# Kernel tuning notes

Measured on AMD Instinct MI355X. Metric: run time of the kernel, lower is better.

Reference implementation:

```python
import jax, jax.numpy as jnp
import numpy as np

KN = 4        # kernel_number
K = 3         # kernel size
CIN = 256
COUT = 256
BN_EPS = 1e-5


def _rotation_matrices(thetas):
    """thetas: [b, n] -> rot mats [b, n, 9, 9] (faithful port of _get_rotation_matrix)."""
    b, n = thetas.shape
    t = thetas.reshape(-1)                      # [b*n]
    x = jnp.cos(t); y = jnp.sin(t)
    a = x - y; bxy = x * y; c = x + y
    z = jnp.zeros_like(t); o = jnp.ones_like(t)
    pos = [
        [a, 1 - a, z, z, z, z, z, z, z],
        [z, x - bxy, bxy, z, 1 - c + bxy, y - bxy, z, z, z],
        [z, z, a, z, z, 1 - a, z, z, z],
        [bxy, y - bxy, z, x - bxy, 1 - c + bxy, z, z, z, z],
        [z, z, z, z, o, z, z, z, z],
        [z, z, z, z, 1 - c + bxy, x - bxy, z, y - bxy, bxy],
        [z, z, z, 1 - a, z, z, a, z, z],
        [z, z, z, y - bxy, 1 - c + bxy, z, bxy, x - bxy, z],
        [z, z, z, z, z, z, z, 1 - a, a],
    ]
    neg = [
        [c, z, z, 1 - c, z, z, z, z, z],
        [-bxy, x + bxy, z, bxy - y, 1 - a - bxy, z, z, z, z],
        [z, 1 - c, c, z, z, z, z, z, z],
        [z, z, z, x + bxy, 1 - a - bxy, z, -bxy, bxy - y, z],
        [z, z, z, z, o, z, z, z, z],
        [z, bxy - y, -bxy, z, 1 - a - bxy, x + bxy, z, z, z],
        [z, z, z, z, z, z, c, 1 - c, z],
        [z, z, z, z, 1 - a - bxy, bxy - y, z, x + bxy, -bxy],
        [z, z, z, z, z, 1 - c, z, z, c],
    ]
    P = jnp.stack([jnp.stack(r, 0) for r in pos], 0)    # [9, 9, b*n]
    N = jnp.stack([jnp.stack(r, 0) for r in neg], 0)    # [9, 9, b*n]
    R = jnp.where(t >= 0, P, N)                          # [9, 9, b*n]
    return R.transpose(2, 0, 1).reshape(b, n, K * K, K * K)


def _rotate_weights(weights, lambdas, thetas):
    """weights [n, Cout, Cin, 3, 3], lambdas/thetas [b, n] -> [b*Cout, Cin, 3, 3]."""
    b, n = thetas.shape
    _, Cout, Cin, _, _ = weights.shape
    rot = _rotation_matrices(thetas) * lambdas[:, :, None, None]   # [b, n, 9, 9]
    rot = rot.transpose(0, 2, 1, 3).reshape(b * K * K, n * K * K)  # [b*9, n*9]
    w = weights.transpose(0, 3, 4, 1, 2).reshape(n * K * K, Cout * Cin)
    w = rot @ w                                                    # [b*9, Cout*Cin]
    w = w.reshape(b, K, K, Cout, Cin).transpose(0, 3, 4, 1, 2)
    return w.reshape(b * Cout, Cin, K, K)


def _forward(x, weight, w_lambda, w_theta, bn_gamma, bn_beta, bn_mean, bn_var):
    b, Cin, H, W = x.shape
    Cout = weight.shape[1]
    # routing: GAP -> linear heads (sigmoid for lambdas, softsign*pi for thetas)
    pooled = x.mean(axis=(2, 3))                        # [b, Cin]
    lambdas = jax.nn.sigmoid(pooled @ w_lambda)         # [b, n]
    thetas = jax.nn.soft_sign(pooled @ w_theta) * jnp.pi  # [b, n]
    # per-sample rotated weights + grouped conv (groups = b)
    rw = _rotate_weights(weight, lambdas, thetas)       # [b*Cout, Cin, 3, 3]
    xr = x.reshape(1, b * Cin, H, W)
    out = jax.lax.conv_general_dilated(
        xr, rw, window_strides=(1, 1), padding=((1, 1), (1, 1)),
        dimension_numbers=('NCHW', 'OIHW', 'NCHW'), feature_group_count=b)
    out = out.reshape(b, Cout, H, W)
    # BatchNorm (inference, running stats) + ReLU
    inv = jax.lax.rsqrt(bn_var + BN_EPS)
    out = (out - bn_mean[None, :, None, None]) * (inv * bn_gamma)[None, :, None, None] \
          + bn_beta[None, :, None, None]
    return jax.nn.relu(out)


def setup_inputs() -> dict:
    key = jax.random.key(0)
    ks = jax.random.split(key, 8)
    B, H, W = 16, 64, 64
    x = jax.random.normal(ks[0], (B, CIN, H, W), dtype=jnp.float32)
    fan_in = CIN * K * K
    weight = jax.random.normal(ks[1], (KN, COUT, CIN, K, K), dtype=jnp.float32) * np.sqrt(2.0 / fan_in)
    w_lambda = jax.random.normal(ks[2], (CIN, KN), dtype=jnp.float32) * np.sqrt(2.0 / CIN)
    w_theta = jax.random.normal(ks[3], (CIN, KN), dtype=jnp.float32) * np.sqrt(2.0 / CIN)
    bn_gamma = jax.random.uniform(ks[4], (COUT,), dtype=jnp.float32, minval=0.5, maxval=1.5)
    bn_beta = jax.random.normal(ks[5], (COUT,), dtype=jnp.float32) * 0.1
    bn_mean = jax.random.normal(ks[6], (COUT,), dtype=jnp.float32) * 0.1
    bn_var = jax.random.uniform(ks[7], (COUT,), dtype=jnp.float32, minval=0.5, maxval=1.5)
    return {'x': x, 'weight': weight, 'w_lambda': w_lambda, 'w_theta': w_theta,
            'bn_gamma': bn_gamma, 'bn_beta': bn_beta, 'bn_mean': bn_mean, 'bn_var': bn_var}


def reference(x, weight, w_lambda, w_theta, bn_gamma, bn_beta, bn_mean, bn_var):
    return _forward(x, weight, w_lambda, w_theta, bn_gamma, bn_beta, bn_mean, bn_var)
```

## Files before the change

### kernel.cpp

```cpp
#include <hip/hip_runtime.h>
#include <math.h>

typedef __bf16  bf16x8 __attribute__((ext_vector_type(8)));
typedef float   f32x4  __attribute__((ext_vector_type(4)));

#define GLD_LDS16(dst, src)                                                      \
    __builtin_amdgcn_global_load_lds(                                            \
        (const __attribute__((address_space(1))) unsigned int*)(src),            \
        (__attribute__((address_space(3))) unsigned int*)(dst), 16, 0, 0)

__global__ __launch_bounds__(256) void transpose_kernel(const float* __restrict__ x,
                                                        __bf16* __restrict__ xT,
                                                        float* __restrict__ pooled) {
    __shared__ unsigned int lp[128][68];
    const int h = blockIdx.x, b = blockIdx.y;
    const int t = threadIdx.x;
    if (h == 0 && b == 0) {
        for (int i = t; i < 4096; i += 256) pooled[i] = 0.f;
    }
    const int w4 = t & 15;
#pragma unroll
    for (int k = 0; k < 8; ++k) {
        int ci2 = k * 16 + (t >> 4);
        int ci  = ci2 * 2;
        const float4 a = *(const float4*)(x + (((size_t)(b * 256 + ci    ) * 64 + h) * 64 + w4 * 4));
        const float4 c = *(const float4*)(x + (((size_t)(b * 256 + ci + 1) * 64 + h) * 64 + w4 * 4));
        union { __bf16 hh[2]; unsigned int u; } p0, p1, p2, p3;
        p0.hh[0] = (__bf16)a.x; p0.hh[1] = (__bf16)c.x;
        p1.hh[0] = (__bf16)a.y; p1.hh[1] = (__bf16)c.y;
        p2.hh[0] = (__bf16)a.z; p2.hh[1] = (__bf16)c.z;
        p3.hh[0] = (__bf16)a.w; p3.hh[1] = (__bf16)c.w;
        uint4 v = {p0.u, p1.u, p2.u, p3.u};
        *(uint4*)&lp[ci2][w4 * 4] = v;
    }
    __syncthreads();
    const int w = t >> 2, q = t & 3;
    __bf16* dst = xT + (((size_t)b * 64 + h) * 64 + w) * 256 + q * 64;
#pragma unroll
    for (int j = 0; j < 8; ++j) {
        int c0 = q * 32 + j * 4;
        uint4 v;
        v.x = lp[c0 + 0][w];
        v.y = lp[c0 + 1][w];
        v.z = lp[c0 + 2][w];
        v.w = lp[c0 + 3][w];
        *(uint4*)(dst + j * 8) = v;
    }
}

__global__ __launch_bounds__(256) void pool_kernel(const __bf16* __restrict__ xT,
                                                   float* __restrict__ pooled) {
    int blk = blockIdx.x;
    int b = blk >> 4, s = blk & 15;
    int t = threadIdx.x;
    int oc  = (t & 31) << 3;
    int hw0 = t >> 5;
    float a8[8];
#pragma unroll
    for (int j = 0; j < 8; j++) a8[j] = 0.f;
    const __bf16* base = xT + (((size_t)b * 4096 + s * 256 + hw0) * 256) + oc;
#pragma unroll 4
    for (int i = 0; i < 32; ++i) {
        bf16x8 v = *(const bf16x8*)(base + (size_t)i * 8 * 256);
#pragma unroll
        for (int j = 0; j < 8; j++) a8[j] += (float)v[j];
    }
    __shared__ float red[256][8];
#pragma unroll
    for (int j = 0; j < 8; j++) red[t][j] = a8[j];
    __syncthreads();
    if (t < 32) {
#pragma unroll
        for (int j = 0; j < 8; j++) {
            float s8 = 0.f;
#pragma unroll
            for (int g = 0; g < 8; g++) s8 += red[g * 32 + t][j];
            atomicAdd(&pooled[b * 256 + t * 8 + j], s8 * (1.f / 4096.f));
        }
    }
}

__global__ __launch_bounds__(64) void routing_kernel(
    const float* __restrict__ pooled, const float* __restrict__ w_lambda,
    const float* __restrict__ w_theta, float* __restrict__ slg) {
    int t = threadIdx.x;
    int b = t >> 2, n = t & 3;
    float zl = 0.f, zt = 0.f;
    for (int ci = 0; ci < 256; ci++) {
        float p = pooled[b * 256 + ci];
        zl += p * w_lambda[ci * 4 + n];
        zt += p * w_theta[ci * 4 + n];
    }
    float lam = 1.f / (1.f + expf(-zl));
    float th  = 3.14159265358979323846f * (zt / (1.f + fabsf(zt)));
    float xc = cosf(th), ys = sinf(th);
    float a = xc - ys, bb = xc * ys, c = xc + ys;
    float R[9][9];
#pragma unroll
    for (int i = 0; i < 9; i++)
#pragma unroll
        for (int j = 0; j < 9; j++) R[i][j] = 0.f;
    if (th >= 0.f) {
        R[0][0] = a;       R[0][1] = 1 - a;
        R[1][1] = xc - bb; R[1][2] = bb;       R[1][4] = 1 - c + bb; R[1][5] = ys - bb;
        R[2][2] = a;       R[2][5] = 1 - a;
        R[3][0] = bb;      R[3][1] = ys - bb;  R[3][3] = xc - bb;    R[3][4] = 1 - c + bb;
        R[4][4] = 1.f;
        R[5][4] = 1 - c + bb; R[5][5] = xc - bb; R[5][7] = ys - bb;  R[5][8] = bb;
        R[6][3] = 1 - a;   R[6][6] = a;
        R[7][3] = ys - bb; R[7][4] = 1 - c + bb; R[7][6] = bb;       R[7][7] = xc - bb;
        R[8][7] = 1 - a;   R[8][8] = a;
    } else {
        R[0][0] = c;       R[0][3] = 1 - c;
        R[1][0] = -bb;     R[1][1] = xc + bb;  R[1][3] = bb - ys;    R[1][4] = 1 - a - bb;
        R[2][1] = 1 - c;   R[2][2] = c;
        R[3][3] = xc + bb; R[3][4] = 1 - a - bb; R[3][6] = -bb;      R[3][7] = bb - ys;
        R[4][4] = 1.f;
        R[5][1] = bb - ys; R[5][2] = -bb;      R[5][4] = 1 - a - bb; R[5][5] = xc + bb;
        R[6][6] = c;       R[6][7] = 1 - c;
        R[7][4] = 1 - a - bb; R[7][5] = bb - ys; R[7][7] = xc + bb;  R[7][8] = -bb;
        R[8][5] = 1 - c;   R[8][8] = c;
    }
    float* o = slg + ((size_t)(b * 4 + n) * 9) * 12;
#pragma unroll
    for (int p = 0; p < 9; p++) {
#pragma unroll
        for (int q = 0; q < 9; q++) o[p * 12 + q] = lam * R[p][q];
        o[p * 12 + 9] = o[p * 12 + 10] = o[p * 12 + 11] = 0.f;
    }
}

__global__ __launch_bounds__(256) void rotw_kernel(
    const float* __restrict__ weight, const float* __restrict__ slg,
    __bf16* __restrict__ rwq) {
    __shared__ __attribute__((aligned(16))) float sl[16][4][9][12];
    __shared__ float wlds[4][2304];
    int co = blockIdx.x;
    int t = threadIdx.x;
#pragma unroll
    for (int n = 0; n < 4; n++) {
        const float* wp = weight + ((size_t)n * 256 + co) * 2304;
        for (int i = t; i < 2304; i += 256) wlds[n][i] = wp[i];
    }
    for (int i = t; i < 1728; i += 256)
        ((float4*)sl)[i] = ((const float4*)slg)[i];
    __syncthreads();
    int ci = t;
    float4 wa[4], wb[4];
    float  wc[4];
#pragma unroll
    for (int n = 0; n < 4; n++) {
        const float* wp = &wlds[n][ci * 9];
        wa[n] = make_float4(wp[0], wp[1], wp[2], wp[3]);
        wb[n] = make_float4(wp[4], wp[5], wp[6], wp[7]);
        wc[n] = wp[8];
    }
    for (int b = 0; b < 16; b++) {
#pragma unroll
        for (int p = 0; p < 9; p++) {
            float s = 0.f;
#pragma unroll
            for (int n = 0; n < 4; n++) {
                float4 sa = *(const float4*)&sl[b][n][p][0];
                float4 sb = *(const float4*)&sl[b][n][p][4];
                float  sc = sl[b][n][p][8];
                s += sa.x * wa[n].x + sa.y * wa[n].y + sa.z * wa[n].z + sa.w * wa[n].w
                   + sb.x * wb[n].x + sb.y * wb[n].y + sb.z * wb[n].z + sb.w * wb[n].w
                   + sc * wc[n];
            }
            rwq[(((size_t)b * 9 + p) * 256 + co) * 256 + ci] = (__bf16)s;
        }
    }
}

__global__ __launch_bounds__(256, 2) void conv_kernel(
    const __bf16* __restrict__ xT, const __bf16* __restrict__ rwq,
    const float* __restrict__ bn_gamma, const float* __restrict__ bn_beta,
    const float* __restrict__ bn_mean,  const float* __restrict__ bn_var,
    float* __restrict__ out) {
    __shared__ __attribute__((aligned(16))) __bf16 xs[10][4][66][8];
    __shared__ __attribute__((aligned(16))) __bf16 as9[9][4][66][8];
    __shared__ float bns[64], bnh[64];

    const int t    = threadIdx.x;
    const int lane = t & 63;
    const int wv   = t >> 6;
    const int l15  = lane & 15;
    const int kq4  = lane >> 4;

    const int lin  = blockIdx.x;
    const int r    = lin & 7;
    const int k    = lin >> 3;
    const int b    = (r << 1) | (k >> 5);
    const int inner = k & 31;
    const int co0  = (inner & 3) << 6;
    const int h0   = (inner >> 2) << 3;

    if (t < 64) {
        float inv = rsqrtf(bn_var[co0 + t] + 1e-5f);
        float sc = bn_gamma[co0 + t] * inv;
        bns[t] = sc;
        bnh[t] = bn_beta[co0 + t] - bn_mean[co0 + t] * sc;
    }

    f32x4 acc[2][4][4];
#pragma unroll
    for (int rr = 0; rr < 2; rr++)
#pragma unroll
        for (int m = 0; m < 4; m++)
#pragma unroll
            for (int n = 0; n < 4; n++) acc[rr][m][n] = (f32x4){0.f, 0.f, 0.f, 0.f};

    const uint4 zero4 = {0u, 0u, 0u, 0u};
    if (t < 40) {
        int rr = t >> 2, kq = t & 3;
        *(uint4*)&xs[rr][kq][0][0]  = zero4;
        *(uint4*)&xs[rr][kq][65][0] = zero4;
    }

    for (int ci0 = 0; ci0 < 256; ci0 += 32) {
        __syncthreads();
#pragma unroll
        for (int u = wv * 10; u < wv * 10 + 10; u++) {
            int rr = u >> 2, kq = u & 3;
            int hh = h0 - 1 + rr;
            if (hh >= 0 && hh < 64) {
                const __bf16* src = xT + (((size_t)(b * 64 + hh) * 64 + lane) * 256 + ci0 + kq * 8);
                GLD_LDS16(&xs[rr][kq][1 + lane][0], src);
            } else {
                *(uint4*)&xs[rr][kq][1 + lane][0] = zero4;
            }
        }
#pragma unroll
        for (int u = wv * 9; u < wv * 9 + 9; u++) {
            int tap = u >> 2, kq = u & 3;
            const __bf16* src = rwq +
                ((((size_t)b * 9 + tap) * 256 + co0 + lane) * 256 + ci0 + kq * 8);
            GLD_LDS16(&as9[tap][kq][lane][0], src);
        }
        __syncthreads();
#pragma unroll
        for (int tap = 0; tap < 9; tap++) {
            const int dh = tap / 3, dw = tap % 3;
            bf16x8 af[4];
#pragma unroll
            for (int m = 0; m < 4; m++)
                af[m] = *(const bf16x8*)&as9[tap][kq4][m * 16 + l15][0];
#pragma unroll
            for (int rr = 0; rr < 2; rr++) {
                const int hl = wv + rr * 4;
#pragma unroll
                for (int nt = 0; nt < 4; nt++) {
                    bf16x8 bfr = *(const bf16x8*)&xs[hl + dh][kq4][nt * 16 + l15 + dw][0];
#pragma unroll
                    for (int m = 0; m < 4; m++)
                        acc[rr][m][nt] = __builtin_amdgcn_mfma_f32_16x16x32_bf16(
                            af[m], bfr, acc[rr][m][nt], 0, 0, 0);
                }
            }
        }
    }

#pragma unroll
    for (int rr = 0; rr < 2; rr++) {
        const int h = h0 + wv + rr * 4;
#pragma unroll
        for (int m = 0; m < 4; m++) {
#pragma unroll
            for (int reg = 0; reg < 4; reg++) {
                int col = m * 16 + kq4 * 4 + reg;
                float sc = bns[col], sh = bnh[col];
                int co = co0 + col;
#pragma unroll
                for (int nt = 0; nt < 4; nt++) {
                    int w = nt * 16 + l15;
                    float v = acc[rr][m][nt][reg] * sc + sh;
                    out[(((size_t)b * 256 + co) * 64 + h) * 64 + w] = v > 0.f ? v : 0.f;
                }
            }
        }
    }
}

extern "C" void kernel_launch(void* const* d_in, const int* in_sizes, int n_in,
                              void* d_out, int out_size, void* d_ws, size_t ws_size,
                              hipStream_t stream) {
    const float* x        = (const float*)d_in[0];
    const float* weight   = (const float*)d_in[1];
    const float* w_lambda = (const float*)d_in[2];
    const float* w_theta  = (const float*)d_in[3];
    const float* bn_gamma = (const float*)d_in[4];
    const float* bn_beta  = (const float*)d_in[5];
    const float* bn_mean  = (const float*)d_in[6];
    const float* bn_var   = (const float*)d_in[7];
    float* out = (float*)d_out;

    char* ws = (char*)d_ws;
    float*  pooled  = (float*)(ws);
    float*  slg     = (float*)(ws + 16384);
    __bf16* xT      = (__bf16*)(ws + 49152);
    __bf16* rwq     = (__bf16*)(ws + 49152 + 33554432);

    transpose_kernel<<<dim3(64, 16), 256, 0, stream>>>(x, xT, pooled);
    pool_kernel<<<256, 256, 0, stream>>>(xT, pooled);
    routing_kernel<<<1, 64, 0, stream>>>(pooled, w_lambda, w_theta, slg);
    rotw_kernel<<<256, 256, 0, stream>>>(weight, slg, rwq);
    conv_kernel<<<512, 256, 0, stream>>>(xT, rwq,
                                         bn_gamma, bn_beta, bn_mean, bn_var, out);
}
```

Before: 268.4 us.

## Fuse global pooling into transpose and parallelize routing across batches

Computes per-row channel partial sums inside the transpose kernel with wavefront shuffles and writes them to a scratch region aliased onto the output buffer. This removes the separate pool kernel, its re-read of the bf16 transposed tensor and its atomics. The routing kernel now runs one block per batch and reduces the partial sums and dot products in parallel instead of using a single 64-thread block. rotw loads weights straight from global memory instead of staging them in LDS. Pooling now sums fp32 inputs rather than bf16 values, and reusing the output buffer as scratch depends on conv overwriting it later.

```diff
diff --git a/kernel.cpp b/kernel.cpp
--- a/kernel.cpp
+++ b/kernel.cpp
@@ -11,20 +11,20 @@
 
 __global__ __launch_bounds__(256) void transpose_kernel(const float* __restrict__ x,
                                                         __bf16* __restrict__ xT,
-                                                        float* __restrict__ pooled) {
+                                                        float* __restrict__ psum) {
     __shared__ unsigned int lp[128][68];
     const int h = blockIdx.x, b = blockIdx.y;
     const int t = threadIdx.x;
-    if (h == 0 && b == 0) {
-        for (int i = t; i < 4096; i += 256) pooled[i] = 0.f;
-    }
     const int w4 = t & 15;
+    float psA[8], psC[8];
 #pragma unroll
     for (int k = 0; k < 8; ++k) {
         int ci2 = k * 16 + (t >> 4);
         int ci  = ci2 * 2;
         const float4 a = *(const float4*)(x + (((size_t)(b * 256 + ci    ) * 64 + h) * 64 + w4 * 4));
         const float4 c = *(const float4*)(x + (((size_t)(b * 256 + ci + 1) * 64 + h) * 64 + w4 * 4));
+        psA[k] = a.x + a.y + a.z + a.w;
+        psC[k] = c.x + c.y + c.z + c.w;
         union { __bf16 hh[2]; unsigned int u; } p0, p1, p2, p3;
         p0.hh[0] = (__bf16)a.x; p0.hh[1] = (__bf16)c.x;
         p1.hh[0] = (__bf16)a.y; p1.hh[1] = (__bf16)c.y;
@@ -32,6 +32,20 @@
         p3.hh[0] = (__bf16)a.w; p3.hh[1] = (__bf16)c.w;
         uint4 v = {p0.u, p1.u, p2.u, p3.u};
         *(uint4*)&lp[ci2][w4 * 4] = v;
+    }
+#pragma unroll
+    for (int k = 0; k < 8; ++k) {
+        float sA = psA[k], sC = psC[k];
+#pragma unroll
+        for (int m = 1; m <= 8; m <<= 1) {
+            sA += __shfl_xor(sA, m, 64);
+            sC += __shfl_xor(sC, m, 64);
+        }
+        if (w4 == 0) {
+            int ci2 = k * 16 + (t >> 4);
+            *(float2*)&psum[(((size_t)b * 64 + h) * 256) + ci2 * 2] =
+                make_float2(sA, sC);
+        }
     }
     __syncthreads();
     const int w = t >> 2, q = t & 3;
@@ -48,85 +62,73 @@
     }
 }
 
-__global__ __launch_bounds__(256) void pool_kernel(const __bf16* __restrict__ xT,
-                                                   float* __restrict__ pooled) {
-    int blk = blockIdx.x;
-    int b = blk >> 4, s = blk & 15;
-    int t = threadIdx.x;
-    int oc  = (t & 31) << 3;
-    int hw0 = t >> 5;
-    float a8[8];
-#pragma unroll
-    for (int j = 0; j < 8; j++) a8[j] = 0.f;
-    const __bf16* base = xT + (((size_t)b * 4096 + s * 256 + hw0) * 256) + oc;
-#pragma unroll 4
-    for (int i = 0; i < 32; ++i) {
-        bf16x8 v = *(const bf16x8*)(base + (size_t)i * 8 * 256);
-#pragma unroll
-        for (int j = 0; j < 8; j++) a8[j] += (float)v[j];
-    }
-    __shared__ float red[256][8];
-#pragma unroll
-    for (int j = 0; j < 8; j++) red[t][j] = a8[j];
+__global__ __launch_bounds__(256) void routing_kernel(
+    const float* __restrict__ psum, const float* __restrict__ w_lambda,
+    const float* __restrict__ w_theta, float* __restrict__ slg) {
+    const int b = blockIdx.x, t = threadIdx.x;
+    float s = 0.f;
+    const float* p = psum + (size_t)b * 16384 + t;
+#pragma unroll 8
+    for (int h = 0; h < 64; ++h) s += p[h * 256];
+    const float pv = s * (1.f / 4096.f);
+    __shared__ float red[8][256];
+    float4 wl = *(const float4*)&w_lambda[t * 4];
+    float4 wt = *(const float4*)&w_theta[t * 4];
+    red[0][t] = pv * wl.x; red[1][t] = pv * wl.y;
+    red[2][t] = pv * wl.z; red[3][t] = pv * wl.w;
+    red[4][t] = pv * wt.x; red[5][t] = pv * wt.y;
+    red[6][t] = pv * wt.z; red[7][t] = pv * wt.w;
     __syncthreads();
-    if (t < 32) {
-#pragma unroll
-        for (int j = 0; j < 8; j++) {
-            float s8 = 0.f;
-#pragma unroll
-            for (int g = 0; g < 8; g++) s8 += red[g * 32 + t][j];
-            atomicAdd(&pooled[b * 256 + t * 8 + j], s8 * (1.f / 4096.f));
-        }
-    }
-}
-
-__global__ __launch_bounds__(64) void routing_kernel(
-    const float* __restrict__ pooled, const float* __restrict__ w_lambda,
-    const float* __restrict__ w_theta, float* __restrict__ slg) {
-    int t = threadIdx.x;
-    int b = t >> 2, n = t & 3;
-    float zl = 0.f, zt = 0.f;
-    for (int ci = 0; ci < 256; ci++) {
-        float p = pooled[b * 256 + ci];
-        zl += p * w_lambda[ci * 4 + n];
-        zt += p * w_theta[ci * 4 + n];
-    }
-    float lam = 1.f / (1.f + expf(-zl));
-    float th  = 3.14159265358979323846f * (zt / (1.f + fabsf(zt)));
-    float xc = cosf(th), ys = sinf(th);
-    float a = xc - ys, bb = xc * ys, c = xc + ys;
-    float R[9][9];
-#pragma unroll
-    for (int i = 0; i < 9; i++)
-#pragma unroll
-        for (int j = 0; j < 9; j++) R[i][j] = 0.f;
-    if (th >= 0.f) {
-        R[0][0] = a;       R[0][1] = 1 - a;
-        R[1][1] = xc - bb; R[1][2] = bb;       R[1][4] = 1 - c + bb; R[1][5] = ys - bb;
-        R[2][2] = a;       R[2][5] = 1 - a;
-        R[3][0] = bb;      R[3][1] = ys - bb;  R[3][3] = xc - bb;    R[3][4] = 1 - c + bb;
-        R[4][4] = 1.f;
-        R[5][4] = 1 - c + bb; R[5][5] = xc - bb; R[5][7] = ys - bb;  R[5][8] = bb;
-        R[6][3] = 1 - a;   R[6][6] = a;
-        R[7][3] = ys - bb; R[7][4] = 1 - c + bb; R[7][6] = bb;       R[7][7] = xc - bb;
-        R[8][7] = 1 - a;   R[8][8] = a;
-    } else {
-        R[0][0] = c;       R[0][3] = 1 - c;
-        R[1][0] = -bb;     R[1][1] = xc + bb;  R[1][3] = bb - ys;    R[1][4] = 1 - a - bb;
-        R[2][1] = 1 - c;   R[2][2] = c;
-        R[3][3] = xc + bb; R[3][4] = 1 - a - bb; R[3][6] = -bb;      R[3][7] = bb - ys;
-        R[4][4] = 1.f;
-        R[5][1] = bb - ys; R[5][2] = -bb;      R[5][4] = 1 - a - bb; R[5][5] = xc + bb;
-        R[6][6] = c;       R[6][7] = 1 - c;
-        R[7][4] = 1 - a - bb; R[7][5] = bb - ys; R[7][7] = xc + bb;  R[7][8] = -bb;
-        R[8][5] = 1 - c;   R[8][8] = c;
-    }
-    float* o = slg + ((size_t)(b * 4 + n) * 9) * 12;
-#pragma unroll
-    for (int p = 0; p < 9; p++) {
-#pragma unroll
-        for (int q = 0; q < 9; q++) o[p * 12 + q] = lam * R[p][q];
-        o[p * 12 + 9] = o[p * 12 + 10] = o[p * 12 + 11] = 0.f;
+    __shared__ float zv[8];
+    const int rrow = t >> 5, i = t & 31;
+    float acc = red[rrow][i]       + red[rrow][i + 32]
+              + red[rrow][i + 64]  + red[rrow][i + 96]
+              + red[rrow][i + 128] + red[rrow][i + 160]
+              + red[rrow][i + 192] + red[rrow][i + 224];
+#pragma unroll
+    for (int m = 16; m >= 1; m >>= 1) acc += __shfl_xor(acc, m, 64);
+    if (i == 0) zv[rrow] = acc;
+    __syncthreads();
+    if (t < 4) {
+        const int n = t;
+        float zl = zv[n], zt = zv[4 + n];
+        float lam = 1.f / (1.f + expf(-zl));
+        float th  = 3.14159265358979323846f * (zt / (1.f + fabsf(zt)));
+        float xc = cosf(th), ys = sinf(th);
+        float a = xc - ys, bb = xc * ys, c = xc + ys;
+        float R[9][9];
+#pragma unroll
+        for (int ii = 0; ii < 9; ii++)
+#pragma unroll
+            for (int jj = 0; jj < 9; jj++) R[ii][jj] = 0.f;
+        if (th >= 0.f) {
+            R[0][0] = a;       R[0][1] = 1 - a;
+            R[1][1] = xc - bb; R[1][2] = bb;       R[1][4] = 1 - c + bb; R[1][5] = ys - bb;
+            R[2][2] = a;       R[2][5] = 1 - a;
+            R[3][0] = bb;      R[3][1] = ys - bb;  R[3][3] = xc - bb;    R[3][4] = 1 - c + bb;
+            R[4][4] = 1.f;
+            R[5][4] = 1 - c + bb; R[5][5] = xc - bb; R[5][7] = ys - bb;  R[5][8] = bb;
+            R[6][3] = 1 - a;   R[6][6] = a;
+            R[7][3] = ys - bb; R[7][4] = 1 - c + bb; R[7][6] = bb;       R[7][7] = xc - bb;
+            R[8][7] = 1 - a;   R[8][8] = a;
+        } else {
+            R[0][0] = c;       R[0][3] = 1 - c;
+            R[1][0] = -bb;     R[1][1] = xc + bb;  R[1][3] = bb - ys;    R[1][4] = 1 - a - bb;
+            R[2][1] = 1 - c;   R[2][2] = c;
+            R[3][3] = xc + bb; R[3][4] = 1 - a - bb; R[3][6] = -bb;      R[3][7] = bb - ys;
+            R[4][4] = 1.f;
+            R[5][1] = bb - ys; R[5][2] = -bb;      R[5][4] = 1 - a - bb; R[5][5] = xc + bb;
+            R[6][6] = c;       R[6][7] = 1 - c;
+            R[7][4] = 1 - a - bb; R[7][5] = bb - ys; R[7][7] = xc + bb;  R[7][8] = -bb;
+            R[8][5] = 1 - c;   R[8][8] = c;
+        }
+        float* o = slg + ((size_t)(b * 4 + n) * 9) * 12;
+#pragma unroll
+        for (int pp = 0; pp < 9; pp++) {
+#pragma unroll
+            for (int q = 0; q < 9; q++) o[pp * 12 + q] = lam * R[pp][q];
+            o[pp * 12 + 9] = o[pp * 12 + 10] = o[pp * 12 + 11] = 0.f;
+        }
     }
 }
 
@@ -134,27 +136,21 @@
     const float* __restrict__ weight, const float* __restrict__ slg,
     __bf16* __restrict__ rwq) {
     __shared__ __attribute__((aligned(16))) float sl[16][4][9][12];
-    __shared__ float wlds[4][2304];
     int co = blockIdx.x;
     int t = threadIdx.x;
-#pragma unroll
-    for (int n = 0; n < 4; n++) {
-        const float* wp = weight + ((size_t)n * 256 + co) * 2304;
-        for (int i = t; i < 2304; i += 256) wlds[n][i] = wp[i];
-    }
     for (int i = t; i < 1728; i += 256)
         ((float4*)sl)[i] = ((const float4*)slg)[i];
-    __syncthreads();
     int ci = t;
     float4 wa[4], wb[4];
     float  wc[4];
 #pragma unroll
     for (int n = 0; n < 4; n++) {
-        const float* wp = &wlds[n][ci * 9];
+        const float* wp = weight + ((size_t)n * 256 + co) * 2304 + (size_t)ci * 9;
         wa[n] = make_float4(wp[0], wp[1], wp[2], wp[3]);
         wb[n] = make_float4(wp[4], wp[5], wp[6], wp[7]);
         wc[n] = wp[8];
     }
+    __syncthreads();
     for (int b = 0; b < 16; b++) {
 #pragma unroll
         for (int p = 0; p < 9; p++) {
@@ -296,14 +292,13 @@
     float* out = (float*)d_out;
 
     char* ws = (char*)d_ws;
-    float*  pooled  = (float*)(ws);
     float*  slg     = (float*)(ws + 16384);
     __bf16* xT      = (__bf16*)(ws + 49152);
     __bf16* rwq     = (__bf16*)(ws + 49152 + 33554432);
-
-    transpose_kernel<<<dim3(64, 16), 256, 0, stream>>>(x, xT, pooled);
-    pool_kernel<<<256, 256, 0, stream>>>(xT, pooled);
-    routing_kernel<<<1, 64, 0, stream>>>(pooled, w_lambda, w_theta, slg);
+    float*  psum    = out;
+
+    transpose_kernel<<<dim3(64, 16), 256, 0, stream>>>(x, xT, psum);
+    routing_kernel<<<16, 256, 0, stream>>>(psum, w_lambda, w_theta, slg);
     rotw_kernel<<<256, 256, 0, stream>>>(weight, slg, rwq);
     conv_kernel<<<512, 256, 0, stream>>>(xT, rwq,
                                          bn_gamma, bn_beta, bn_mean, bn_var, out);
```

Measured after the change: 239.9 us. -10.6%, faster.
